# Kernel optimization log

Measured on AMD Instinct MI355X. Metric: run time of the kernel, lower is better.

Reference implementation:

```python
import jax, jax.numpy as jnp
import numpy as np

B, Wd, C, H, F = 48, 88, 256, 32, 1024
NH_SELF, NH_CROSS = 8, 8


def _ln(x, g, b, eps=1e-5):
    mu = x.mean(-1, keepdims=True)
    var = ((x - mu) ** 2).mean(-1, keepdims=True)
    return (x - mu) / jnp.sqrt(var + eps) * g + b


def setup_inputs() -> dict:
    key = jax.random.key(0)
    ks = jax.random.split(key, 16)
    s = 0.02  # weight init scale
    d = {
        'pooled_features': jax.random.normal(ks[0], (B, Wd, C), jnp.float32),
        'features': jax.random.normal(ks[1], (B, C, H, Wd), jnp.float32),
        'self_pe': jax.random.normal(ks[2], (Wd, C), jnp.float32),
        'cross_pe': jax.random.normal(ks[3], (H, C), jnp.float32),
    }
    # LayerNorm params
    for n in ['ln_qs', 'ln_vs', 'ln_qc', 'ln_kv', 'ln_vc', 'ln_ffn']:
        d[n + '_g'] = jnp.ones((C,), jnp.float32)
        d[n + '_b'] = jnp.zeros((C,), jnp.float32)
    # attention projections (stored [in,out]; y = x @ W + b)
    names = ['Wq_s', 'Wk_s', 'Wv_s', 'Wp_s', 'Wq_c', 'Wk_c', 'Wv_c', 'Wp_c']
    for i, n in enumerate(names):
        d[n] = jax.random.normal(ks[4 + i], (C, C), jnp.float32) * s
    for n in ['bq_s', 'bv_s', 'bp_s', 'bq_c', 'bv_c', 'bp_c']:
        d[n] = jnp.zeros((C,), jnp.float32)
    # FFN
    d['W1'] = jax.random.normal(ks[12], (C, F), jnp.float32) * s
    d['b1'] = jnp.zeros((F,), jnp.float32)
    d['W2'] = jax.random.normal(ks[13], (F, C), jnp.float32) * s
    d['b2'] = jnp.zeros((C,), jnp.float32)
    return d


def reference(pooled_features, features, self_pe, cross_pe,
              ln_qs_g, ln_qs_b, ln_vs_g, ln_vs_b,
              ln_qc_g, ln_qc_b, ln_kv_g, ln_kv_b, ln_vc_g, ln_vc_b,
              ln_ffn_g, ln_ffn_b,
              Wq_s, bq_s, Wk_s, Wv_s, bv_s, Wp_s, bp_s,
              Wq_c, bq_c, Wk_c, Wv_c, bv_c, Wp_c, bp_c,
              W1, b1, W2, b2):
    b, w, c = pooled_features.shape
    h = features.shape[2]
    ds = c // NH_SELF
    dc = c // NH_CROSS

    # ---- cross attention first (op_order='cross_first', with_pe=True) ----
    xq = pooled_features                                  # [B,W,C]
    qn = _ln(xq, ln_qc_g, ln_qc_b)
    kv = jnp.transpose(features, (0, 3, 2, 1))            # [B,W,H,C]
    kn = _ln(kv + cross_pe[None, None], ln_kv_g, ln_kv_b)
    vn = _ln(kv, ln_vc_g, ln_vc_b)
    q = (qn @ Wq_c + bq_c).reshape(b, w, NH_CROSS, dc)    # query len 1 per column
    k = (kn @ Wk_c).reshape(b, w, h, NH_CROSS, dc)
    v = (vn @ Wv_c + bv_c).reshape(b, w, h, NH_CROSS, dc)
    attn = jnp.einsum('bwhd,bwkhd->bwhk', q, k) * (dc ** -0.5)
    attn = jax.nn.softmax(attn, axis=-1)
    out = jnp.einsum('bwhk,bwkhd->bwhd', attn, v).reshape(b, w, c)
    x = out @ Wp_c + bp_c + xq

    # ---- self attention over width tokens ----
    qn = _ln(x + self_pe[None], ln_qs_g, ln_qs_b)
    vn = _ln(x, ln_vs_g, ln_vs_b)
    q = (qn @ Wq_s + bq_s).reshape(b, w, NH_SELF, ds)
    k = (qn @ Wk_s).reshape(b, w, NH_SELF, ds)
    v = (vn @ Wv_s + bv_s).reshape(b, w, NH_SELF, ds)
    attn = jnp.einsum('bnhd,bmhd->bhnm', q, k) * (ds ** -0.5)
    attn = jax.nn.softmax(attn, axis=-1)
    out = jnp.einsum('bhnm,bmhd->bnhd', attn, v).reshape(b, w, c)
    x = out @ Wp_s + bp_s + x

    # ---- FFN (mmcv FFN, num_fcs=2, GELU, identity residual) ----
    hdn = _ln(x, ln_ffn_g, ln_ffn_b)
    hdn = jax.nn.gelu(hdn @ W1 + b1, approximate=False) @ W2 + b2
    return x + hdn
```

## Files before the change

### kernel.cpp

```cpp
#include <hip/hip_runtime.h>
#include <math.h>

#define B_   48
#define W_   88
#define C_   256
#define H_   32
#define F_   1024
#define BW_  (B_ * W_)
#define BWH_ (B_ * W_ * H_)
#define HW_  (H_ * W_)

typedef float  f32x4  __attribute__((ext_vector_type(4)));
typedef __bf16 bf16x8 __attribute__((ext_vector_type(8)));

__device__ __forceinline__ unsigned short f2bf(float f) {
  union { float f; unsigned int u; } v; v.f = f;
  unsigned int r = v.u + 0x7FFFu + ((v.u >> 16) & 1u);
  return (unsigned short)(r >> 16);
}
__device__ __forceinline__ float bf2f(unsigned short h) {
  union { unsigned int u; float f; } v; v.u = ((unsigned int)h) << 16;
  return v.f;
}
__device__ __forceinline__ unsigned int pack2(float a, float b) {
  return (unsigned int)f2bf(a) | ((unsigned int)f2bf(b) << 16);
}

__global__ __launch_bounds__(256) void prep_all(
    const float* __restrict__ Wq_s, const float* __restrict__ Wk_s,
    const float* __restrict__ Wv_s, const float* __restrict__ Wp_s,
    const float* __restrict__ W1, const float* __restrict__ W2,
    const float* __restrict__ Wq_c, const float* __restrict__ Wk_c,
    const float* __restrict__ Wv_c, const float* __restrict__ Wp_c,
    const float* __restrict__ bq_s, const float* __restrict__ bv_s,
    const float* __restrict__ bq_c, const float* __restrict__ bv_c,
    const float* __restrict__ bp_c,
    const float* __restrict__ pooled,
    const float* __restrict__ ln_qc_g, const float* __restrict__ ln_qc_b,
    const float* __restrict__ cross_pe,
    unsigned short* __restrict__ wqkvs, unsigned short* __restrict__ wps,
    unsigned short* __restrict__ w1t, unsigned short* __restrict__ w2t,
    unsigned short* __restrict__ mqk, unsigned short* __restrict__ mvp,
    float* __restrict__ bqk, float* __restrict__ bvp,
    float* __restrict__ bqkvs, unsigned short* __restrict__ qn_c,
    float* __restrict__ pes) {
  __shared__ float smem[256 * 33 + 4 * 33];
  int blk = blockIdx.x, t = threadIdx.x;

  if (blk < 768) {
    const float* src; unsigned short* dst; int Cc, R, tile;
    if (blk < 64)       { src = Wq_s; dst = wqkvs;          Cc = 256;  R = 256;  tile = blk; }
    else if (blk < 128) { src = Wk_s; dst = wqkvs + 65536;  Cc = 256;  R = 256;  tile = blk - 64; }
    else if (blk < 192) { src = Wv_s; dst = wqkvs + 131072; Cc = 256;  R = 256;  tile = blk - 128; }
    else if (blk < 256) { src = Wp_s; dst = wps;            Cc = 256;  R = 256;  tile = blk - 192; }
    else if (blk < 512) { src = W1;   dst = w1t;            Cc = 1024; R = 256;  tile = blk - 256; }
    else                { src = W2;   dst = w2t;            Cc = 256;  R = 1024; tile = blk - 512; }
    int tcn = Cc >> 5;
    int tr = tile / tcn, tc = tile % tcn;
    float (*lds)[33] = (float(*)[33])smem;
    int r = t >> 3, c4 = (t & 7) * 4;
    float4 v = *(const float4*)(src + (size_t)(tr * 32 + r) * Cc + tc * 32 + c4);
    lds[r][c4 + 0] = v.x; lds[r][c4 + 1] = v.y; lds[r][c4 + 2] = v.z; lds[r][c4 + 3] = v.w;
    __syncthreads();
    int rd = t >> 3, cd4 = (t & 7) * 4;
    unsigned int u0 = pack2(lds[cd4 + 0][rd], lds[cd4 + 1][rd]);
    unsigned int u1 = pack2(lds[cd4 + 2][rd], lds[cd4 + 3][rd]);
    uint2 u; u.x = u0; u.y = u1;
    *(uint2*)(dst + (size_t)(tc * 32 + rd) * R + tr * 32 + cd4) = u;
  } else if (blk < 1280) {
    int lb = blk - 768;
    int h = lb >> 6, cb = lb & 63;
    float (*wq)[33] = (float(*)[33])smem;
    float (*wk)[33] = (float(*)[33])(smem + 256 * 33);
#pragma unroll
    for (int p = 0; p < 8; p++) {
      int dp = (t >> 3) + 32 * p, d4 = (t & 7) * 4;
      float4 v = *(const float4*)(Wq_c + (size_t)dp * 256 + 32 * h + d4);
      wq[dp][d4 + 0] = v.x; wq[dp][d4 + 1] = v.y; wq[dp][d4 + 2] = v.z; wq[dp][d4 + 3] = v.w;
    }
    if (t < 128) {
      int c_l = t >> 5, dd = t & 31;
      wk[c_l][dd] = Wk_c[(size_t)(cb * 4 + c_l) * 256 + 32 * h + dd];
    }
    __syncthreads();
    const float scale = 0.17677669529663689f;
    int c_l = t >> 6, ln = t & 63;
    int n = 256 * h + cb * 4 + c_l;
#pragma unroll
    for (int j = 0; j < 4; j++) {
      int dp = ln + 64 * j;
      float acc = 0.f;
#pragma unroll
      for (int dd = 0; dd < 32; dd++) acc += wq[dp][dd] * wk[c_l][dd];
      mqk[(size_t)n * 256 + dp] = f2bf(acc * scale);
    }
    if (ln == 0) {
      float bb = 0.f;
#pragma unroll
      for (int dd = 0; dd < 32; dd++) bb += bq_c[32 * h + dd] * wk[c_l][dd];
      bqk[n] = bb * scale;
    }
  } else if (blk < 1792) {
    int lb = blk - 1280;
    int h = lb >> 6, db = lb & 63;
    float (*wv)[33] = (float(*)[33])smem;
    float (*wp)[33] = (float(*)[33])(smem + 256 * 33);
#pragma unroll
    for (int p = 0; p < 8; p++) {
      int c = (t >> 3) + 32 * p, d4 = (t & 7) * 4;
      float4 v = *(const float4*)(Wv_c + (size_t)c * 256 + 32 * h + d4);
      wv[c][d4 + 0] = v.x; wv[c][d4 + 1] = v.y; wv[c][d4 + 2] = v.z; wv[c][d4 + 3] = v.w;
    }
    if (t < 128) {
      int d_l = t >> 5, dd = t & 31;
      wp[d_l][dd] = Wp_c[(size_t)(32 * h + dd) * 256 + db * 4 + d_l];
    }
    __syncthreads();
    int d_l = t >> 6, ln = t & 63;
    int d = db * 4 + d_l;
#pragma unroll
    for (int j = 0; j < 4; j++) {
      int c = ln + 64 * j;
      float acc = 0.f;
#pragma unroll
      for (int dd = 0; dd < 32; dd++) acc += wv[c][dd] * wp[d_l][dd];
      mvp[(size_t)d * 2048 + 256 * h + c] = f2bf(acc);
    }
  } else if (blk == 1792) {
    float acc = bp_c[t];
    for (int dp = 0; dp < 256; dp++) acc += bv_c[dp] * Wp_c[(size_t)dp * 256 + t];
    bvp[t] = acc;
    bqkvs[t] = bq_s[t]; bqkvs[256 + t] = 0.f; bqkvs[512 + t] = bv_s[t];
  } else if (blk < 6017) {
    int row = blk - 1793, c = t;
    float v = pooled[(size_t)row * C_ + c];
    float s1 = v, s2 = v * v;
#pragma unroll
    for (int m = 32; m > 0; m >>= 1) {
      s1 += __shfl_xor(s1, m, 64); s2 += __shfl_xor(s2, m, 64);
    }
    float* red = smem;
    int wave = c >> 6;
    if ((c & 63) == 0) { red[wave] = s1; red[4 + wave] = s2; }
    __syncthreads();
    s1 = red[0] + red[1] + red[2] + red[3];
    s2 = red[4] + red[5] + red[6] + red[7];
    float mu = s1 * (1.f / C_);
    float rs = rsqrtf(s2 * (1.f / C_) - mu * mu + 1e-5f);
    qn_c[(size_t)row * C_ + c] = f2bf((v - mu) * rs * ln_qc_g[c] + ln_qc_b[c]);
  } else {
    int h = t >> 3, seg = t & 7;
    const float* pr = cross_pe + (size_t)h * 256 + seg * 32;
    float s1 = 0.f, s2 = 0.f;
#pragma unroll
    for (int i = 0; i < 32; i++) { float v = pr[i]; s1 += v; s2 += v * v; }
    s1 += __shfl_xor(s1, 1, 8); s2 += __shfl_xor(s2, 1, 8);
    s1 += __shfl_xor(s1, 2, 8); s2 += __shfl_xor(s2, 2, 8);
    s1 += __shfl_xor(s1, 4, 8); s2 += __shfl_xor(s2, 4, 8);
    if (seg == 0) { pes[2 * h] = s1; pes[2 * h + 1] = s2; }
  }
}

__global__ __launch_bounds__(256, 2) void cross_fused(
    const float* __restrict__ features, const float* __restrict__ cross_pe,
    const unsigned short* __restrict__ qt_g,
    const float* __restrict__ g_kv, const float* __restrict__ b_kv,
    const float* __restrict__ g_vc, const float* __restrict__ b_vc,
    const float* __restrict__ pes,
    unsigned short* __restrict__ ctx_g) {
  __shared__ __attribute__((aligned(16))) unsigned short qtl[8 * 2048];
  __shared__ __attribute__((aligned(16))) float stage[2 * 8 * 268];
  const int p = blockIdx.x;
  const int xcd = p & 7, slot = p >> 3;
  const int b = xcd + 8 * (slot / 11);
  const int w0 = (slot % 11) * 8;
  const int t = threadIdx.x;
  const int bw0 = b * 88 + w0;

  for (int i = t; i < 2048; i += 256) {
    int r = i >> 8, c = (i & 255) << 3;
    *(uint4*)&qtl[r * 2048 + c] = *(const uint4*)(qt_g + (size_t)(bw0 + r) * 2048 + c);
  }

  const int w = t >> 5, c8 = t & 31, cbase = c8 << 3;
  float gk[8], bk[8], gv[8], bv[8];
  {
    float4 u0 = *(const float4*)(g_kv + cbase), u1 = *(const float4*)(g_kv + cbase + 4);
    gk[0]=u0.x; gk[1]=u0.y; gk[2]=u0.z; gk[3]=u0.w; gk[4]=u1.x; gk[5]=u1.y; gk[6]=u1.z; gk[7]=u1.w;
    u0 = *(const float4*)(b_kv + cbase); u1 = *(const float4*)(b_kv + cbase + 4);
    bk[0]=u0.x; bk[1]=u0.y; bk[2]=u0.z; bk[3]=u0.w; bk[4]=u1.x; bk[5]=u1.y; bk[6]=u1.z; bk[7]=u1.w;
    u0 = *(const float4*)(g_vc + cbase); u1 = *(const float4*)(g_vc + cbase + 4);
    gv[0]=u0.x; gv[1]=u0.y; gv[2]=u0.z; gv[3]=u0.w; gv[4]=u1.x; gv[5]=u1.y; gv[6]=u1.z; gv[7]=u1.w;
    u0 = *(const float4*)(b_vc + cbase); u1 = *(const float4*)(b_vc + cbase + 4);
    bv[0]=u0.x; bv[1]=u0.y; bv[2]=u0.z; bv[3]=u0.w; bv[4]=u1.x; bv[5]=u1.y; bv[6]=u1.z; bv[7]=u1.w;
  }
  float acc[8][8];
#pragma unroll
  for (int hd = 0; hd < 8; hd++)
#pragma unroll
    for (int i = 0; i < 8; i++) acc[hd][i] = 0.f;
  float l[8];
#pragma unroll
  for (int hd = 0; hd < 8; hd++) l[hd] = 0.f;

  const float* fbase = features + (size_t)b * (C_ * HW_) + w0;
  float4 x0 = *(const float4*)(fbase + (size_t)t * HW_);
  float4 x1 = *(const float4*)(fbase + (size_t)t * HW_ + 4);
  float4 y0 = *(const float4*)(fbase + (size_t)t * HW_ + 88);
  float4 y1 = *(const float4*)(fbase + (size_t)t * HW_ + 92);

#pragma unroll 2
  for (int h = 0; h < 32; ++h) {
    float* st = stage + (h & 1) * (8 * 268);
    st[t] = x0.x; st[268 + t] = x0.y; st[536 + t] = x0.z; st[804 + t] = x0.w;
    st[1072 + t] = x1.x; st[1340 + t] = x1.y; st[1608 + t] = x1.z; st[1876 + t] = x1.w;
    asm volatile("s_waitcnt lgkmcnt(0)" ::: "memory");
    __builtin_amdgcn_s_barrier();
    asm volatile("" ::: "memory");
    if (h < 30) {
      x0 = *(const float4*)(fbase + (size_t)t * HW_ + (h + 2) * 88);
      x1 = *(const float4*)(fbase + (size_t)t * HW_ + (h + 2) * 88 + 4);
    }
    const float* sr = st + w * 268 + cbase;
    float4 v0 = *(const float4*)(sr);
    float4 v1 = *(const float4*)(sr + 4);
    float vls[8] = {v0.x, v0.y, v0.z, v0.w, v1.x, v1.y, v1.z, v1.w};
    float4 q0 = *(const float4*)(cross_pe + h * 256 + cbase);
    float4 q1 = *(const float4*)(cross_pe + h * 256 + cbase + 4);
    float pe8[8] = {q0.x, q0.y, q0.z, q0.w, q1.x, q1.y, q1.z, q1.w};
    float s1 = 0.f, s2 = 0.f, sp = 0.f;
#pragma unroll
    for (int i = 0; i < 8; i++) {
      s1 += vls[i]; s2 += vls[i] * vls[i]; sp += vls[i] * pe8[i];
    }
#pragma unroll
    for (int m = 1; m < 32; m <<= 1) {
      s1 += __shfl_xor(s1, m, 32);
      s2 += __shfl_xor(s2, m, 32);
      sp += __shfl_xor(sp, m, 32);
    }
    float mu_v = s1 * (1.f / 256.f);
    float rs_v = rsqrtf(s2 * (1.f / 256.f) - mu_v * mu_v + 1e-5f);
    float mu_k = (s1 + pes[2 * h]) * (1.f / 256.f);
    float rs_k = rsqrtf((s2 + 2.f * sp + pes[2 * h + 1]) * (1.f / 256.f)
                        - mu_k * mu_k + 1e-5f);
    float kn8[8], vn8[8];
#pragma unroll
    for (int i = 0; i < 8; i++) {
      vn8[i] = (vls[i] - mu_v) * rs_v * gv[i] + bv[i];
      kn8[i] = (vls[i] + pe8[i] - mu_k) * rs_k * gk[i] + bk[i];
    }
    float sc[8];
#pragma unroll
    for (int hd = 0; hd < 8; hd++) {
      bf16x8 q = *(const bf16x8*)&qtl[w * 2048 + hd * 256 + cbase];
      float a = 0.f;
#pragma unroll
      for (int i = 0; i < 8; i++) a += kn8[i] * (float)q[i];
      sc[hd] = a;
    }
#pragma unroll
    for (int m = 1; m < 32; m <<= 1) {
#pragma unroll
      for (int hd = 0; hd < 8; hd++) sc[hd] += __shfl_xor(sc[hd], m, 32);
    }
#pragma unroll
    for (int hd = 0; hd < 8; hd++) {
      float e = __expf(sc[hd]);
      l[hd] += e;
#pragma unroll
      for (int i = 0; i < 8; i++) acc[hd][i] += e * vn8[i];
    }
    float4 t0 = x0, t1 = x1;
    x0 = y0; x1 = y1;
    y0 = t0; y1 = t1;
  }
  unsigned short* orow = ctx_g + (size_t)(bw0 + w) * 2048 + cbase;
#pragma unroll
  for (int hd = 0; hd < 8; hd++) {
    float inv = 1.f / l[hd];
    unsigned short pk[8];
#pragma unroll
    for (int i = 0; i < 8; i++) pk[i] = f2bf(acc[hd][i] * inv);
    *(uint4*)(orow + hd * 256) = *(uint4*)pk;
  }
}

__global__ __launch_bounds__(256) void ln_rows(
    const float* __restrict__ x,
    const float* __restrict__ g, const float* __restrict__ bta,
    unsigned short* __restrict__ out) {
  int row = blockIdx.x, c = threadIdx.x;
  float v = x[(size_t)row * C_ + c];
  float s1 = v, s2 = v * v;
#pragma unroll
  for (int m = 32; m > 0; m >>= 1) {
    s1 += __shfl_xor(s1, m, 64);
    s2 += __shfl_xor(s2, m, 64);
  }
  __shared__ float red[8];
  int wave = c >> 6;
  if ((c & 63) == 0) { red[wave] = s1; red[4 + wave] = s2; }
  __syncthreads();
  s1 = red[0] + red[1] + red[2] + red[3];
  s2 = red[4] + red[5] + red[6] + red[7];
  float mu = s1 * (1.f / C_);
  float rs = rsqrtf(s2 * (1.f / C_) - mu * mu + 1e-5f);
  out[(size_t)row * C_ + c] = f2bf((v - mu) * rs * g[c] + bta[c]);
}

__global__ __launch_bounds__(256) void ln_dual(
    const float* __restrict__ x, const float* __restrict__ pe,
    const float* __restrict__ g1, const float* __restrict__ b1a,
    const float* __restrict__ g2, const float* __restrict__ b2a,
    unsigned short* __restrict__ out1, unsigned short* __restrict__ out2) {
  int row = blockIdx.x, c = threadIdx.x;
  float v = x[(size_t)row * C_ + c];
  float vp = v + pe[(size_t)(row % 88) * C_ + c];
  float s1 = v, s2 = v * v, t1 = vp, t2 = vp * vp;
#pragma unroll
  for (int m = 32; m > 0; m >>= 1) {
    s1 += __shfl_xor(s1, m, 64); s2 += __shfl_xor(s2, m, 64);
    t1 += __shfl_xor(t1, m, 64); t2 += __shfl_xor(t2, m, 64);
  }
  __shared__ float red[16];
  int wave = c >> 6;
  if ((c & 63) == 0) {
    red[wave] = s1; red[4 + wave] = s2; red[8 + wave] = t1; red[12 + wave] = t2;
  }
  __syncthreads();
  s1 = red[0] + red[1] + red[2] + red[3];
  s2 = red[4] + red[5] + red[6] + red[7];
  t1 = red[8] + red[9] + red[10] + red[11];
  t2 = red[12] + red[13] + red[14] + red[15];
  float mu = s1 * (1.f / C_), rs = rsqrtf(s2 * (1.f / C_) - mu * mu + 1e-5f);
  float mup = t1 * (1.f / C_), rsp = rsqrtf(t2 * (1.f / C_) - mup * mup + 1e-5f);
  out1[(size_t)row * C_ + c] = f2bf((vp - mup) * rsp * g1[c] + b1a[c]);
  out2[(size_t)row * C_ + c] = f2bf((v - mu) * rs * g2[c] + b2a[c]);
}

__global__ __launch_bounds__(256) void gemm_bt(
    const unsigned short* __restrict__ A, const unsigned short* __restrict__ Bt,
    int M, int N, int K,
    const float* __restrict__ bias, const float* __restrict__ resid,
    float* __restrict__ outF, unsigned short* __restrict__ outB, int act_gelu) {
  __shared__ __attribute__((aligned(16))) unsigned short As[64][32];
  __shared__ __attribute__((aligned(16))) unsigned short Bs[64][32];
  const int tiles_n = N >> 6;
  const int bm = blockIdx.x / tiles_n;
  const int bn = blockIdx.x % tiles_n;
  const int tid = threadIdx.x;
  const int wave = tid >> 6, lane = tid & 63;
  const int quad = lane >> 4, lr = lane & 15;
  const int wm = (wave >> 1) << 5, wn = (wave & 1) << 5;
  const int lrow = tid >> 2;
  const int lcol = (tid & 3) << 3;
  const size_t a_base = (size_t)(bm * 64 + lrow) * K + lcol;
  const size_t b_base = (size_t)(bn * 64 + lrow) * K + lcol;
  f32x4 acc[2][2] = {};
  uint4 areg = *(const uint4*)(A + a_base);
  uint4 breg = *(const uint4*)(Bt + b_base);
  for (int k0 = 0; k0 < K; k0 += 32) {
    *(uint4*)&As[lrow][lcol] = areg;
    *(uint4*)&Bs[lrow][lcol] = breg;
    __syncthreads();
    if (k0 + 32 < K) {
      areg = *(const uint4*)(A + a_base + k0 + 32);
      breg = *(const uint4*)(Bt + b_base + k0 + 32);
    }
    bf16x8 af0 = *(const bf16x8*)&As[wm + lr][quad << 3];
    bf16x8 af1 = *(const bf16x8*)&As[wm + 16 + lr][quad << 3];
    bf16x8 bf0 = *(const bf16x8*)&Bs[wn + lr][quad << 3];
    bf16x8 bf1 = *(const bf16x8*)&Bs[wn + 16 + lr][quad << 3];
    acc[0][0] = __builtin_amdgcn_mfma_f32_16x16x32_bf16(af0, bf0, acc[0][0], 0, 0, 0);
    acc[0][1] = __builtin_amdgcn_mfma_f32_16x16x32_bf16(af0, bf1, acc[0][1], 0, 0, 0);
    acc[1][0] = __builtin_amdgcn_mfma_f32_16x16x32_bf16(af1, bf0, acc[1][0], 0, 0, 0);
    acc[1][1] = __builtin_amdgcn_mfma_f32_16x16x32_bf16(af1, bf1, acc[1][1], 0, 0, 0);
    __syncthreads();
  }
#pragma unroll
  for (int i = 0; i < 2; i++)
#pragma unroll
    for (int j = 0; j < 2; j++)
#pragma unroll
      for (int rr = 0; rr < 4; rr++) {
        int row = bm * 64 + wm + i * 16 + quad * 4 + rr;
        int col = bn * 64 + wn + j * 16 + lr;
        float val = acc[i][j][rr];
        if (bias) val += bias[col];
        if (act_gelu) val = 0.5f * val * (1.f + erff(val * 0.70710678118654752f));
        if (resid) val += resid[(size_t)row * N + col];
        if (outF) outF[(size_t)row * N + col] = val;
        else outB[(size_t)row * N + col] = f2bf(val);
      }
}

__global__ __launch_bounds__(256) void gemm_bt_st(
    const unsigned short* __restrict__ A, const unsigned short* __restrict__ Bt,
    int M, int N, int K, int ldc,
    const float* __restrict__ bias, float* __restrict__ outF) {
  __shared__ __attribute__((aligned(16))) unsigned short As[64][32];
  __shared__ __attribute__((aligned(16))) unsigned short Bs[64][32];
  const int tiles_n = N >> 6;
  const int bm = blockIdx.x / tiles_n;
  const int bn = blockIdx.x % tiles_n;
  const int tid = threadIdx.x;
  const int wave = tid >> 6, lane = tid & 63;
  const int quad = lane >> 4, lr = lane & 15;
  const int wm = (wave >> 1) << 5, wn = (wave & 1) << 5;
  const int lrow = tid >> 2;
  const int lcol = (tid & 3) << 3;
  const size_t a_base = (size_t)(bm * 64 + lrow) * K + lcol;
  const size_t b_base = (size_t)(bn * 64 + lrow) * K + lcol;
  f32x4 acc[2][2] = {};
  uint4 areg = *(const uint4*)(A + a_base);
  uint4 breg = *(const uint4*)(Bt + b_base);
  for (int k0 = 0; k0 < K; k0 += 32) {
    *(uint4*)&As[lrow][lcol] = areg;
    *(uint4*)&Bs[lrow][lcol] = breg;
    __syncthreads();
    if (k0 + 32 < K) {
      areg = *(const uint4*)(A + a_base + k0 + 32);
      breg = *(const uint4*)(Bt + b_base + k0 + 32);
    }
    bf16x8 af0 = *(const bf16x8*)&As[wm + lr][quad << 3];
    bf16x8 af1 = *(const bf16x8*)&As[wm + 16 + lr][quad << 3];
    bf16x8 bf0 = *(const bf16x8*)&Bs[wn + lr][quad << 3];
    bf16x8 bf1 = *(const bf16x8*)&Bs[wn + 16 + lr][quad << 3];
    acc[0][0] = __builtin_amdgcn_mfma_f32_16x16x32_bf16(af0, bf0, acc[0][0], 0, 0, 0);
    acc[0][1] = __builtin_amdgcn_mfma_f32_16x16x32_bf16(af0, bf1, acc[0][1], 0, 0, 0);
    acc[1][0] = __builtin_amdgcn_mfma_f32_16x16x32_bf16(af1, bf0, acc[1][0], 0, 0, 0);
    acc[1][1] = __builtin_amdgcn_mfma_f32_16x16x32_bf16(af1, bf1, acc[1][1], 0, 0, 0);
    __syncthreads();
  }
#pragma unroll
  for (int i = 0; i < 2; i++)
#pragma unroll
    for (int j = 0; j < 2; j++)
#pragma unroll
      for (int rr = 0; rr < 4; rr++) {
        int row = bm * 64 + wm + i * 16 + quad * 4 + rr;
        int col = bn * 64 + wn + j * 16 + lr;
        outF[(size_t)row * ldc + col] = acc[i][j][rr] + bias[col];
      }
}

__global__ __launch_bounds__(192) void self_attn3(
    const float* __restrict__ qkv, unsigned short* __restrict__ out) {
  int b = blockIdx.x >> 3;
  int h = blockIdx.x & 7;
  int t = threadIdx.x;
  __shared__ float kl[88][33];
  __shared__ float vl[88][33];
  for (int i = t; i < 704; i += 192) {
    int m = i >> 3, d4 = (i & 7) << 2;
    float4 kv4 = *(const float4*)(qkv + (size_t)(b * 88 + m) * 768 + 256 + h * 32 + d4);
    float4 vv4 = *(const float4*)(qkv + (size_t)(b * 88 + m) * 768 + 512 + h * 32 + d4);
    kl[m][d4 + 0] = kv4.x; kl[m][d4 + 1] = kv4.y; kl[m][d4 + 2] = kv4.z; kl[m][d4 + 3] = kv4.w;
    vl[m][d4 + 0] = vv4.x; vl[m][d4 + 1] = vv4.y; vl[m][d4 + 2] = vv4.z; vl[m][d4 + 3] = vv4.w;
  }
  __syncthreads();
  int r = t >> 1, dh = t & 1;
  if (r < 88) {
    const float* qrow = qkv + (size_t)(b * 88 + r) * 768 + h * 32;
    float qr[32];
#pragma unroll
    for (int g = 0; g < 8; g++) {
      float4 q4 = *(const float4*)(qrow + g * 4);
      qr[g * 4 + 0] = q4.x; qr[g * 4 + 1] = q4.y; qr[g * 4 + 2] = q4.z; qr[g * 4 + 3] = q4.w;
    }
    float sreg[44];
    float mx = -1e30f;
    int m0 = dh * 44;
    for (int mi = 0; mi < 44; mi++) {
      const float* krow = kl[m0 + mi];
      float s = 0.f;
#pragma unroll
      for (int d = 0; d < 32; d++) s += qr[d] * krow[d];
      s *= 0.17677669529663689f;
      sreg[mi] = s;
      mx = fmaxf(mx, s);
    }
    mx = fmaxf(mx, __shfl_xor(mx, 1, 64));
    float sum = 0.f;
    for (int mi = 0; mi < 44; mi++) { float e = __expf(sreg[mi] - mx); sreg[mi] = e; sum += e; }
    sum += __shfl_xor(sum, 1, 64);
    float inv = 1.f / sum;
    float o[32];
#pragma unroll
    for (int d = 0; d < 32; d++) o[d] = 0.f;
    for (int mi = 0; mi < 44; mi++) {
      float p = sreg[mi] * inv;
      const float* vrow = vl[m0 + mi];
#pragma unroll
      for (int d = 0; d < 32; d++) o[d] += p * vrow[d];
    }
#pragma unroll
    for (int d = 0; d < 32; d++) o[d] += __shfl_xor(o[d], 1, 64);
    unsigned short* orow = out + (size_t)(b * 88 + r) * 256 + h * 32 + dh * 16;
    uint4 u0, u1;
    int d0 = dh * 16;
    u0.x = pack2(o[d0 + 0], o[d0 + 1]);  u0.y = pack2(o[d0 + 2], o[d0 + 3]);
    u0.z = pack2(o[d0 + 4], o[d0 + 5]);  u0.w = pack2(o[d0 + 6], o[d0 + 7]);
    u1.x = pack2(o[d0 + 8], o[d0 + 9]);  u1.y = pack2(o[d0 + 10], o[d0 + 11]);
    u1.z = pack2(o[d0 + 12], o[d0 + 13]); u1.w = pack2(o[d0 + 14], o[d0 + 15]);
    *(uint4*)(orow) = u0;
    *(uint4*)(orow + 8) = u1;
  }
}

extern "C" void kernel_launch(void* const* d_in, const int* in_sizes, int n_in,
                              void* d_out, int out_size, void* d_ws, size_t ws_size,
                              hipStream_t stream) {
  (void)in_sizes; (void)n_in; (void)out_size; (void)ws_size;
  const float* pooled   = (const float*)d_in[0];
  const float* features = (const float*)d_in[1];
  const float* self_pe  = (const float*)d_in[2];
  const float* cross_pe = (const float*)d_in[3];
  const float* ln_qs_g = (const float*)d_in[4],  *ln_qs_b = (const float*)d_in[5];
  const float* ln_vs_g = (const float*)d_in[6],  *ln_vs_b = (const float*)d_in[7];
  const float* ln_qc_g = (const float*)d_in[8],  *ln_qc_b = (const float*)d_in[9];
  const float* ln_kv_g = (const float*)d_in[10], *ln_kv_b = (const float*)d_in[11];
  const float* ln_vc_g = (const float*)d_in[12], *ln_vc_b = (const float*)d_in[13];
  const float* ln_ffn_g = (const float*)d_in[14], *ln_ffn_b = (const float*)d_in[15];
  const float* Wq_s = (const float*)d_in[16], *Wk_s = (const float*)d_in[17];
  const float* Wv_s = (const float*)d_in[18], *Wp_s = (const float*)d_in[19];
  const float* Wq_c = (const float*)d_in[20], *Wk_c = (const float*)d_in[21];
  const float* Wv_c = (const float*)d_in[22], *Wp_c = (const float*)d_in[23];
  const float* bq_s = (const float*)d_in[24], *bv_s = (const float*)d_in[25];
  const float* bp_s = (const float*)d_in[26], *bq_c = (const float*)d_in[27];
  const float* bv_c = (const float*)d_in[28], *bp_c = (const float*)d_in[29];
  const float* W1 = (const float*)d_in[30], *b1 = (const float*)d_in[31];
  const float* W2 = (const float*)d_in[32], *b2 = (const float*)d_in[33];
  float* outp = (float*)d_out;
  char* ws = (char*)d_ws;

  size_t off = 0;
  auto alloc = [&](size_t bytes) { size_t o = off; off = (off + bytes + 255) & ~(size_t)255; return o; };
  size_t QT  = alloc((size_t)BW_ * 2048 * 2);
  size_t CTX = alloc((size_t)BW_ * 2048 * 2);
  size_t MQK = alloc((size_t)2048 * 256 * 2);
  size_t MVP = alloc((size_t)256 * 2048 * 2);
  size_t BQK = alloc(2048 * 4);
  size_t BVP = alloc(256 * 4);
  size_t WQKVS = alloc((size_t)768 * 256 * 2);
  size_t BQKVS = alloc(768 * 4);
  size_t WPS = alloc(65536 * 2);
  size_t W1T = alloc(262144 * 2), W2T = alloc(262144 * 2);
  size_t QN_C = alloc((size_t)BW_ * C_ * 2);
  size_t PES  = alloc(64 * 4);
  size_t X1    = alloc((size_t)BW_ * C_ * 4);
  size_t QN_S  = alloc((size_t)BW_ * C_ * 2);
  size_t VN_S  = alloc((size_t)BW_ * C_ * 2);
  size_t QKV_S = alloc((size_t)BW_ * 768 * 4);
  size_t S_O   = alloc((size_t)BW_ * C_ * 2);
  size_t X2    = alloc((size_t)BW_ * C_ * 4);
  size_t FFN   = alloc((size_t)BW_ * C_ * 2);
  size_t H1    = alloc((size_t)BW_ * F_ * 2);

  unsigned short* qt   = (unsigned short*)(ws + QT);
  unsigned short* ctx  = (unsigned short*)(ws + CTX);
  unsigned short* mqk  = (unsigned short*)(ws + MQK);
  unsigned short* mvp  = (unsigned short*)(ws + MVP);
  float* bqk = (float*)(ws + BQK);
  float* bvp = (float*)(ws + BVP);
  unsigned short* wqkvs = (unsigned short*)(ws + WQKVS);
  float* bqkvs = (float*)(ws + BQKVS);
  unsigned short* wps = (unsigned short*)(ws + WPS);
  unsigned short* w1t = (unsigned short*)(ws + W1T), *w2t = (unsigned short*)(ws + W2T);
  unsigned short* qn_c = (unsigned short*)(ws + QN_C);
  float* pes = (float*)(ws + PES);
  float*          x1   = (float*)(ws + X1);
  unsigned short* qn_s = (unsigned short*)(ws + QN_S);
  unsigned short* vn_s = (unsigned short*)(ws + VN_S);
  float* qkv_s = (float*)(ws + QKV_S);
  unsigned short* s_o  = (unsigned short*)(ws + S_O);
  float*          x2   = (float*)(ws + X2);
  unsigned short* ffn_n = (unsigned short*)(ws + FFN);
  unsigned short* h1    = (unsigned short*)(ws + H1);

  prep_all<<<6018, 256, 0, stream>>>(
      Wq_s, Wk_s, Wv_s, Wp_s, W1, W2, Wq_c, Wk_c, Wv_c, Wp_c,
      bq_s, bv_s, bq_c, bv_c, bp_c, pooled, ln_qc_g, ln_qc_b, cross_pe,
      wqkvs, wps, w1t, w2t, mqk, mvp, bqk, bvp, bqkvs, qn_c, pes);

  gemm_bt<<<(BW_ / 64) * (2048 / 64), 256, 0, stream>>>(qn_c, mqk, BW_, 2048, 256,
      bqk, nullptr, nullptr, qt, 0);

  cross_fused<<<528, 256, 0, stream>>>(features, cross_pe, qt,
      ln_kv_g, ln_kv_b, ln_vc_g, ln_vc_b, pes, ctx);

  gemm_bt<<<(BW_ / 64) * (C_ / 64), 256, 0, stream>>>(ctx, mvp, BW_, C_, 2048,
      bvp, pooled, x1, nullptr, 0);

  ln_dual<<<BW_, 256, 0, stream>>>(x1, self_pe, ln_qs_g, ln_qs_b,
                                   ln_vs_g, ln_vs_b, qn_s, vn_s);

  gemm_bt_st<<<(BW_ / 64) * (512 / 64), 256, 0, stream>>>(qn_s, wqkvs, BW_, 512, 256,
      768, bqkvs, qkv_s);
  gemm_bt_st<<<(BW_ / 64) * (256 / 64), 256, 0, stream>>>(vn_s, wqkvs + 131072, BW_, 256, 256,
      768, bqkvs + 512, qkv_s + 512);

  self_attn3<<<B_ * 8, 192, 0, stream>>>(qkv_s, s_o);

  gemm_bt<<<(BW_ / 64) * (C_ / 64), 256, 0, stream>>>(s_o, wps, BW_, C_, C_,
      bp_s, x1, x2, nullptr, 0);

  ln_rows<<<BW_, 256, 0, stream>>>(x2, ln_ffn_g, ln_ffn_b, ffn_n);
  gemm_bt<<<(BW_ / 64) * (F_ / 64), 256, 0, stream>>>(ffn_n, w1t, BW_, F_, C_,
      b1, nullptr, nullptr, h1, 1);
  gemm_bt<<<(BW_ / 64) * (C_ / 64), 256, 0, stream>>>(h1, w2t, BW_, C_, F_,
      b2, x2, outp, nullptr, 0);
}
```

Before: 516.0 us.

## Fold LayerNorm affine into query/value algebra in cross attention, halve block size

Measured after the change: 504.4 us. 1.02x faster.

```diff
diff --git a/kernel.cpp b/kernel.cpp
--- a/kernel.cpp
+++ b/kernel.cpp
@@ -161,65 +161,83 @@
   }
 }
 
-__global__ __launch_bounds__(256, 2) void cross_fused(
+__global__ __launch_bounds__(128, 2) void cross_fused(
     const float* __restrict__ features, const float* __restrict__ cross_pe,
     const unsigned short* __restrict__ qt_g,
     const float* __restrict__ g_kv, const float* __restrict__ b_kv,
     const float* __restrict__ g_vc, const float* __restrict__ b_vc,
     const float* __restrict__ pes,
     unsigned short* __restrict__ ctx_g) {
-  __shared__ __attribute__((aligned(16))) unsigned short qtl[8 * 2048];
-  __shared__ __attribute__((aligned(16))) float stage[2 * 8 * 268];
+  __shared__ __attribute__((aligned(16))) float stage[2 * 4 * 268];
   const int p = blockIdx.x;
   const int xcd = p & 7, slot = p >> 3;
-  const int b = xcd + 8 * (slot / 11);
-  const int w0 = (slot % 11) * 8;
+  const int b = xcd + 8 * (slot / 22);
+  const int w0 = (slot % 22) * 4;
   const int t = threadIdx.x;
   const int bw0 = b * 88 + w0;
-
-  for (int i = t; i < 2048; i += 256) {
-    int r = i >> 8, c = (i & 255) << 3;
-    *(uint4*)&qtl[r * 2048 + c] = *(const uint4*)(qt_g + (size_t)(bw0 + r) * 2048 + c);
-  }
-
   const int w = t >> 5, c8 = t & 31, cbase = c8 << 3;
-  float gk[8], bk[8], gv[8], bv[8];
+
+  float qg[8][8], Qg[8], Qb[8];
   {
+    float gk8[8], bk8[8];
     float4 u0 = *(const float4*)(g_kv + cbase), u1 = *(const float4*)(g_kv + cbase + 4);
-    gk[0]=u0.x; gk[1]=u0.y; gk[2]=u0.z; gk[3]=u0.w; gk[4]=u1.x; gk[5]=u1.y; gk[6]=u1.z; gk[7]=u1.w;
+    gk8[0]=u0.x; gk8[1]=u0.y; gk8[2]=u0.z; gk8[3]=u0.w;
+    gk8[4]=u1.x; gk8[5]=u1.y; gk8[6]=u1.z; gk8[7]=u1.w;
     u0 = *(const float4*)(b_kv + cbase); u1 = *(const float4*)(b_kv + cbase + 4);
-    bk[0]=u0.x; bk[1]=u0.y; bk[2]=u0.z; bk[3]=u0.w; bk[4]=u1.x; bk[5]=u1.y; bk[6]=u1.z; bk[7]=u1.w;
-    u0 = *(const float4*)(g_vc + cbase); u1 = *(const float4*)(g_vc + cbase + 4);
-    gv[0]=u0.x; gv[1]=u0.y; gv[2]=u0.z; gv[3]=u0.w; gv[4]=u1.x; gv[5]=u1.y; gv[6]=u1.z; gv[7]=u1.w;
-    u0 = *(const float4*)(b_vc + cbase); u1 = *(const float4*)(b_vc + cbase + 4);
-    bv[0]=u0.x; bv[1]=u0.y; bv[2]=u0.z; bv[3]=u0.w; bv[4]=u1.x; bv[5]=u1.y; bv[6]=u1.z; bv[7]=u1.w;
-  }
-  float acc[8][8];
-#pragma unroll
-  for (int hd = 0; hd < 8; hd++)
-#pragma unroll
-    for (int i = 0; i < 8; i++) acc[hd][i] = 0.f;
-  float l[8];
-#pragma unroll
-  for (int hd = 0; hd < 8; hd++) l[hd] = 0.f;
+    bk8[0]=u0.x; bk8[1]=u0.y; bk8[2]=u0.z; bk8[3]=u0.w;
+    bk8[4]=u1.x; bk8[5]=u1.y; bk8[6]=u1.z; bk8[7]=u1.w;
+    const unsigned short* qrow = qt_g + (size_t)(bw0 + w) * 2048 + cbase;
+#pragma unroll
+    for (int hd = 0; hd < 8; hd++) {
+      bf16x8 qv = *(const bf16x8*)(qrow + hd * 256);
+      float sg = 0.f, sb = 0.f;
+#pragma unroll
+      for (int i = 0; i < 8; i++) {
+        float qf = (float)qv[i];
+        qg[hd][i] = qf * gk8[i];
+        sg += qg[hd][i];
+        sb += qf * bk8[i];
+      }
+      Qg[hd] = sg; Qb[hd] = sb;
+    }
+#pragma unroll
+    for (int m = 1; m < 32; m <<= 1) {
+#pragma unroll
+      for (int hd = 0; hd < 8; hd++) {
+        Qg[hd] += __shfl_xor(Qg[hd], m, 32);
+        Qb[hd] += __shfl_xor(Qb[hd], m, 32);
+      }
+    }
+  }
+
+  float accA[8][8];
+  float accB[8], l[8];
+#pragma unroll
+  for (int hd = 0; hd < 8; hd++) {
+    accB[hd] = 0.f; l[hd] = 0.f;
+#pragma unroll
+    for (int i = 0; i < 8; i++) accA[hd][i] = 0.f;
+  }
 
   const float* fbase = features + (size_t)b * (C_ * HW_) + w0;
   float4 x0 = *(const float4*)(fbase + (size_t)t * HW_);
-  float4 x1 = *(const float4*)(fbase + (size_t)t * HW_ + 4);
+  float4 x1 = *(const float4*)(fbase + (size_t)(t + 128) * HW_);
   float4 y0 = *(const float4*)(fbase + (size_t)t * HW_ + 88);
-  float4 y1 = *(const float4*)(fbase + (size_t)t * HW_ + 92);
+  float4 y1 = *(const float4*)(fbase + (size_t)(t + 128) * HW_ + 88);
 
 #pragma unroll 2
   for (int h = 0; h < 32; ++h) {
-    float* st = stage + (h & 1) * (8 * 268);
-    st[t] = x0.x; st[268 + t] = x0.y; st[536 + t] = x0.z; st[804 + t] = x0.w;
-    st[1072 + t] = x1.x; st[1340 + t] = x1.y; st[1608 + t] = x1.z; st[1876 + t] = x1.w;
+    float* st = stage + (h & 1) * (4 * 268);
+    st[0 * 268 + t] = x0.x; st[1 * 268 + t] = x0.y;
+    st[2 * 268 + t] = x0.z; st[3 * 268 + t] = x0.w;
+    st[0 * 268 + 128 + t] = x1.x; st[1 * 268 + 128 + t] = x1.y;
+    st[2 * 268 + 128 + t] = x1.z; st[3 * 268 + 128 + t] = x1.w;
     asm volatile("s_waitcnt lgkmcnt(0)" ::: "memory");
     __builtin_amdgcn_s_barrier();
     asm volatile("" ::: "memory");
     if (h < 30) {
       x0 = *(const float4*)(fbase + (size_t)t * HW_ + (h + 2) * 88);
-      x1 = *(const float4*)(fbase + (size_t)t * HW_ + (h + 2) * 88 + 4);
+      x1 = *(const float4*)(fbase + (size_t)(t + 128) * HW_ + (h + 2) * 88);
     }
     const float* sr = st + w * 268 + cbase;
     float4 v0 = *(const float4*)(sr);
@@ -229,59 +247,65 @@
     float4 q1 = *(const float4*)(cross_pe + h * 256 + cbase + 4);
     float pe8[8] = {q0.x, q0.y, q0.z, q0.w, q1.x, q1.y, q1.z, q1.w};
     float s1 = 0.f, s2 = 0.f, sp = 0.f;
+    float vp[8];
 #pragma unroll
     for (int i = 0; i < 8; i++) {
-      s1 += vls[i]; s2 += vls[i] * vls[i]; sp += vls[i] * pe8[i];
+      float v = vls[i];
+      vp[i] = v + pe8[i];
+      s1 += v; s2 += v * v; sp += v * pe8[i];
+    }
+    float S[8];
+#pragma unroll
+    for (int hd = 0; hd < 8; hd++) {
+      float a = 0.f;
+#pragma unroll
+      for (int i = 0; i < 8; i++) a += qg[hd][i] * vp[i];
+      S[hd] = a;
     }
 #pragma unroll
     for (int m = 1; m < 32; m <<= 1) {
       s1 += __shfl_xor(s1, m, 32);
       s2 += __shfl_xor(s2, m, 32);
       sp += __shfl_xor(sp, m, 32);
+#pragma unroll
+      for (int hd = 0; hd < 8; hd++) S[hd] += __shfl_xor(S[hd], m, 32);
     }
     float mu_v = s1 * (1.f / 256.f);
     float rs_v = rsqrtf(s2 * (1.f / 256.f) - mu_v * mu_v + 1e-5f);
     float mu_k = (s1 + pes[2 * h]) * (1.f / 256.f);
     float rs_k = rsqrtf((s2 + 2.f * sp + pes[2 * h + 1]) * (1.f / 256.f)
                         - mu_k * mu_k + 1e-5f);
-    float kn8[8], vn8[8];
-#pragma unroll
-    for (int i = 0; i < 8; i++) {
-      vn8[i] = (vls[i] - mu_v) * rs_v * gv[i] + bv[i];
-      kn8[i] = (vls[i] + pe8[i] - mu_k) * rs_k * gk[i] + bk[i];
-    }
-    float sc[8];
 #pragma unroll
     for (int hd = 0; hd < 8; hd++) {
-      bf16x8 q = *(const bf16x8*)&qtl[w * 2048 + hd * 256 + cbase];
-      float a = 0.f;
-#pragma unroll
-      for (int i = 0; i < 8; i++) a += kn8[i] * (float)q[i];
-      sc[hd] = a;
-    }
-#pragma unroll
-    for (int m = 1; m < 32; m <<= 1) {
-#pragma unroll
-      for (int hd = 0; hd < 8; hd++) sc[hd] += __shfl_xor(sc[hd], m, 32);
-    }
-#pragma unroll
-    for (int hd = 0; hd < 8; hd++) {
-      float e = __expf(sc[hd]);
+      float sc = rs_k * (S[hd] - mu_k * Qg[hd]) + Qb[hd];
+      float e = __expf(sc);
+      float er = e * rs_v;
       l[hd] += e;
-#pragma unroll
-      for (int i = 0; i < 8; i++) acc[hd][i] += e * vn8[i];
+      accB[hd] += er * mu_v;
+#pragma unroll
+      for (int i = 0; i < 8; i++) accA[hd][i] += er * vls[i];
     }
     float4 t0 = x0, t1 = x1;
     x0 = y0; x1 = y1;
     y0 = t0; y1 = t1;
   }
+  float gv8[8], bv8[8];
+  {
+    float4 u0 = *(const float4*)(g_vc + cbase), u1 = *(const float4*)(g_vc + cbase + 4);
+    gv8[0]=u0.x; gv8[1]=u0.y; gv8[2]=u0.z; gv8[3]=u0.w;
+    gv8[4]=u1.x; gv8[5]=u1.y; gv8[6]=u1.z; gv8[7]=u1.w;
+    u0 = *(const float4*)(b_vc + cbase); u1 = *(const float4*)(b_vc + cbase + 4);
+    bv8[0]=u0.x; bv8[1]=u0.y; bv8[2]=u0.z; bv8[3]=u0.w;
+    bv8[4]=u1.x; bv8[5]=u1.y; bv8[6]=u1.z; bv8[7]=u1.w;
+  }
   unsigned short* orow = ctx_g + (size_t)(bw0 + w) * 2048 + cbase;
 #pragma unroll
   for (int hd = 0; hd < 8; hd++) {
     float inv = 1.f / l[hd];
     unsigned short pk[8];
 #pragma unroll
-    for (int i = 0; i < 8; i++) pk[i] = f2bf(acc[hd][i] * inv);
+    for (int i = 0; i < 8; i++)
+      pk[i] = f2bf(gv8[i] * (accA[hd][i] - accB[hd]) * inv + bv8[i]);
     *(uint4*)(orow + hd * 256) = *(uint4*)pk;
   }
 }
@@ -587,7 +611,7 @@
   gemm_bt<<<(BW_ / 64) * (2048 / 64), 256, 0, stream>>>(qn_c, mqk, BW_, 2048, 256,
       bqk, nullptr, nullptr, qt, 0);
 
-  cross_fused<<<528, 256, 0, stream>>>(features, cross_pe, qt,
+  cross_fused<<<1056, 128, 0, stream>>>(features, cross_pe, qt,
       ln_kv_g, ln_kv_b, ln_vc_g, ln_vc_b, pes, ctx);
 
   gemm_bt<<<(BW_ / 64) * (C_ / 64), 256, 0, stream>>>(ctx, mvp, BW_, C_, 2048,
```
